# Kernel tuning notes

Measured on AMD Instinct MI355X. Metric: run time of the kernel, lower is better.

The kernel has to match this reference:

```python
import jax, jax.numpy as jnp
import numpy as np

B, K, NPER, Fin, Fmem, H = 64, 16, 256, 256, 128, 8
LN_EPS = 1e-5


def _build_edges():
    # each memory slot (src) attends over all K slots + NPER nodes of its batch elem
    BK = B * K
    dest_chunks = []
    for b in range(B):
        dest_b = np.concatenate([b * K + np.arange(K), BK + b * NPER + np.arange(NPER)])
        dest_chunks.append(np.tile(dest_b, K))
    dest = np.concatenate(dest_chunks).astype(np.int32)
    src = np.repeat(np.arange(BK), K + NPER).astype(np.int32)
    return src, dest


def setup_inputs() -> dict:
    key = jax.random.key(0)
    ks = jax.random.split(key, 16)
    N = B * NPER
    BK = B * K
    src, dest = _build_edges()
    s = 0.02
    return {
        'x': jax.random.normal(ks[0], (N, Fin), jnp.float32),
        'memory': jax.random.normal(ks[1], (BK, Fmem), jnp.float32),
        'Wp': jax.random.normal(ks[2], (Fin, Fmem), jnp.float32) * s,
        'bp': jnp.zeros((Fmem,), jnp.float32),
        'Wqkv': jax.random.normal(ks[3], (Fmem, 3 * Fmem), jnp.float32) * s,  # bias=False
        'ln1_g': jnp.ones((Fmem,), jnp.float32),
        'ln1_b': jnp.zeros((Fmem,), jnp.float32),
        'W1': jax.random.normal(ks[4], (Fmem, Fmem), jnp.float32) * s,
        'b1': jnp.zeros((Fmem,), jnp.float32),
        'W2': jax.random.normal(ks[5], (Fmem, Fmem), jnp.float32) * s,
        'b2': jnp.zeros((Fmem,), jnp.float32),
        'ln2_g': jnp.ones((Fmem,), jnp.float32),
        'ln2_b': jnp.zeros((Fmem,), jnp.float32),
        'Wg': jax.random.normal(ks[6], (2 * Fmem, 2 * Fmem), jnp.float32) * s,
        'bg': jnp.zeros((2 * Fmem,), jnp.float32),
        'src': jnp.asarray(src),
        'dest': jnp.asarray(dest),
    }


def layer_norm(x, g, b):
    mu = x.mean(-1, keepdims=True)
    var = ((x - mu) ** 2).mean(-1, keepdims=True)
    return (x - mu) * jax.lax.rsqrt(var + LN_EPS) * g + b


def reference(x, memory, Wp, bp, Wqkv, ln1_g, ln1_b, W1, b1, W2, b2,
              ln2_g, ln2_b, Wg, bg, src, dest):
    BK, F = memory.shape
    Fh = F // H
    # input projection and concat [memory; x]
    xp = x @ Wp + bp                               # [N, Fmem]
    mem_cat = jnp.concatenate([memory, xp], 0)     # [BK + N, Fmem]
    # qkv projection (no bias), Fqk = Fv = Fmem
    q, k, v = jnp.split(mem_cat @ Wqkv, 3, axis=-1)
    q = (q * (float(Fh) ** -0.5)).reshape(-1, H, Fh)
    k = k.reshape(-1, H, Fh)
    v = v.reshape(-1, H, Fh)
    # per-edge attention scores
    aw = jnp.einsum('ehf,ehf->eh', q[src], k[dest])          # [E, H]
    # scatter softmax over src segments
    m = jax.ops.segment_max(aw, src, num_segments=BK)
    e = jnp.exp(aw - m[src])
    z = jax.ops.segment_sum(e, src, num_segments=BK)
    p = e / z[src]                                            # [E, H]
    # weighted scatter-sum aggregation
    out = jax.ops.segment_sum(p[:, :, None] * v[dest], src, num_segments=BK)
    out = out.reshape(BK, F)
    # residual + LN, MLP, residual + LN
    mem_tmp = layer_norm(memory + out, ln1_g, ln1_b)
    mem_update = jax.nn.relu(mem_tmp @ W1 + b1) @ W2 + b2
    mem_update = layer_norm(mem_tmp + mem_update, ln2_g, ln2_b)
    # feature-level LSTM-style gating
    gate = jnp.concatenate([memory, mem_update], -1) @ Wg + bg
    f, i = jnp.split(gate, 2, axis=-1)
    new_mem = memory * jax.nn.sigmoid(f) + mem_update * jax.nn.sigmoid(i)
    return new_mem  # original returns (output, memory) with output is memory
```

## Files before the change

kernel.cpp:

```cpp
#include <hip/hip_runtime.h>
#include <hip/hip_bf16.h>

#define B_    64
#define K_    16
#define NPER_ 256
#define FIN_  256
#define F_    128
#define H_    8
#define N_    (B_ * NPER_)
#define BK_   (B_ * K_)
#define KV_   (K_ + NPER_)
#define LN_EPS_ 1e-5f

__device__ __forceinline__ float bf2f(unsigned short u) {
    union { unsigned u; float f; } c; c.u = ((unsigned)u) << 16; return c.f;
}
template<bool BF>
__device__ __forceinline__ float ldT(const void* p, long i) {
    if (BF) return bf2f(((const unsigned short*)p)[i]);
    else    return ((const float*)p)[i];
}
template<bool BF>
__device__ __forceinline__ float2 ld2T(const void* p, long i) {
    if (BF) {
        const unsigned u = *(const unsigned*)((const unsigned short*)p + i);
        return make_float2(bf2f((unsigned short)(u & 0xffffu)),
                           bf2f((unsigned short)(u >> 16)));
    } else {
        return *(const float2*)((const float*)p + i);
    }
}
template<bool BF>
__device__ __forceinline__ float4 ld4T(const void* p, long i) {
    if (BF) {
        const uint2 u = *(const uint2*)((const unsigned short*)p + i);
        return make_float4(bf2f((unsigned short)(u.x & 0xffffu)),
                           bf2f((unsigned short)(u.x >> 16)),
                           bf2f((unsigned short)(u.y & 0xffffu)),
                           bf2f((unsigned short)(u.y >> 16)));
    } else {
        return *(const float4*)((const float*)p + i);
    }
}
template<bool BF>
__device__ __forceinline__ void stT(void* p, long i, float v) {
    if (BF) ((__hip_bfloat16*)p)[i] = __float2bfloat16(v);
    else    ((float*)p)[i] = v;
}
__device__ __forceinline__ bool is_bf(const unsigned* probe) {
    return probe[0] != 0x3F800000u;
}

#define R1 32

template<bool BF>
__device__ __forceinline__ void stage_wp(const void* Wp, int c, float* dst, int t) {
    const long base = (long)c * 2048;
    *(float4*)(dst + 4 * t)        = ld4T<BF>(Wp, base + 4 * t);
    *(float4*)(dst + 1024 + 4 * t) = ld4T<BF>(Wp, base + 1024 + 4 * t);
}
template<bool BF>
__device__ __forceinline__ void stage_wkv(const void* Wqkv, int c, float* dst, int t) {
    #pragma unroll
    for (int p = 0; p < 2; ++p) {
        const int d = p * 1024 + 4 * t;
        const int rr = d >> 8, cc = d & 255;
        *(float4*)(dst + d) = ld4T<BF>(Wqkv, (long)(c * 8 + rr) * 384 + 128 + cc);
    }
}

template<bool BF>
__device__ void nodes_kv_body(const void* x, const void* Wp, const void* bp,
                              const void* Wqkv, float* kx, float* vx,
                              float* xs, float* xps, float* wb0, float* wb1) {
    const int t = threadIdx.x;
    const long row0 = (long)blockIdx.x * R1;
    #pragma unroll
    for (int p = 0; p < 8; ++p) {
        const int d = p * 1024 + 4 * t;
        *(float4*)(xs + d) = ld4T<BF>(x, row0 * FIN_ + d);
    }
    stage_wp<BF>(Wp, 0, wb0, t);
    __syncthreads();
    const int j2 = (t & 63) * 2;
    const int r0 = (t >> 6) * 8;
    {
        float a0[8], a1[8];
        #pragma unroll
        for (int r = 0; r < 8; ++r) { a0[r] = 0.f; a1[r] = 0.f; }
        for (int c = 0; c < 16; ++c) {
            const float* w = (c & 1) ? wb1 : wb0;
            if (c < 15) stage_wp<BF>(Wp, c + 1, (c & 1) ? wb0 : wb1, t);
            #pragma unroll
            for (int g = 0; g < 16; g += 4) {
                const float2 w0 = *(const float2*)(w + (g + 0) * F_ + j2);
                const float2 w1 = *(const float2*)(w + (g + 1) * F_ + j2);
                const float2 w2 = *(const float2*)(w + (g + 2) * F_ + j2);
                const float2 w3 = *(const float2*)(w + (g + 3) * F_ + j2);
                #pragma unroll
                for (int r = 0; r < 8; ++r) {
                    const float4 x4 = *(const float4*)(xs + (r0 + r) * FIN_ + c * 16 + g);
                    a0[r] += x4.x * w0.x + x4.y * w1.x + x4.z * w2.x + x4.w * w3.x;
                    a1[r] += x4.x * w0.y + x4.y * w1.y + x4.z * w2.y + x4.w * w3.y;
                }
            }
            __syncthreads();
        }
        stage_wkv<BF>(Wqkv, 0, wb0, t);
        const float2 bb = ld2T<BF>(bp, j2);
        #pragma unroll
        for (int r = 0; r < 8; ++r)
            *(float2*)(xps + (r0 + r) * F_ + j2) = make_float2(a0[r] + bb.x, a1[r] + bb.y);
    }
    __syncthreads();
    {
        float b0[8], b1[8], c0a[8], c1a[8];
        #pragma unroll
        for (int r = 0; r < 8; ++r) { b0[r] = b1[r] = c0a[r] = c1a[r] = 0.f; }
        for (int c = 0; c < 16; ++c) {
            const float* w = (c & 1) ? wb1 : wb0;
            if (c < 15) stage_wkv<BF>(Wqkv, c + 1, (c & 1) ? wb0 : wb1, t);
            #pragma unroll
            for (int g = 0; g < 8; g += 4) {
                const float2 wk0 = *(const float2*)(w + (g + 0) * 256 + j2);
                const float2 wk1 = *(const float2*)(w + (g + 1) * 256 + j2);
                const float2 wk2 = *(const float2*)(w + (g + 2) * 256 + j2);
                const float2 wk3 = *(const float2*)(w + (g + 3) * 256 + j2);
                const float2 wv0 = *(const float2*)(w + (g + 0) * 256 + 128 + j2);
                const float2 wv1 = *(const float2*)(w + (g + 1) * 256 + 128 + j2);
                const float2 wv2 = *(const float2*)(w + (g + 2) * 256 + 128 + j2);
                const float2 wv3 = *(const float2*)(w + (g + 3) * 256 + 128 + j2);
                #pragma unroll
                for (int r = 0; r < 8; ++r) {
                    const float4 p4 = *(const float4*)(xps + (r0 + r) * F_ + c * 8 + g);
                    b0[r]  += p4.x * wk0.x + p4.y * wk1.x + p4.z * wk2.x + p4.w * wk3.x;
                    b1[r]  += p4.x * wk0.y + p4.y * wk1.y + p4.z * wk2.y + p4.w * wk3.y;
                    c0a[r] += p4.x * wv0.x + p4.y * wv1.x + p4.z * wv2.x + p4.w * wv3.x;
                    c1a[r] += p4.x * wv0.y + p4.y * wv1.y + p4.z * wv2.y + p4.w * wv3.y;
                }
            }
            __syncthreads();
        }
        #pragma unroll
        for (int r = 0; r < 8; ++r) {
            const long g = (row0 + r0 + r) * F_;
            *(float2*)(kx + g + j2) = make_float2(b0[r], b1[r]);
            *(float2*)(vx + g + j2) = make_float2(c0a[r], c1a[r]);
        }
    }
}
__global__ __launch_bounds__(256) void k_nodes_kv(const void* x, const void* Wp,
        const void* bp, const void* Wqkv, const unsigned* probe,
        float* kx, float* vx) {
    __shared__ float xs[R1 * FIN_];
    __shared__ float xps[R1 * F_];
    __shared__ float wb0[2048];
    __shared__ float wb1[2048];
    if (is_bf(probe)) nodes_kv_body<true >(x, Wp, bp, Wqkv, kx, vx, xs, xps, wb0, wb1);
    else              nodes_kv_body<false>(x, Wp, bp, Wqkv, kx, vx, xs, xps, wb0, wb1);
}

#define KPAD 20
template<bool BF>
__device__ void attn_body(const void* mem, const void* Wqkv,
                          const float* kx, const float* vx, float* attn_out,
                          float* ms, float* qh, float* kh, float* vh, float* S) {
    const int b = blockIdx.x >> 3, h = blockIdx.x & 7;
    const int t = threadIdx.x;
    #pragma unroll
    for (int p = 0; p < 2; ++p) {
        const int d = p * 1024 + 4 * t;
        *(float4*)(ms + d) = ld4T<BF>(mem, (long)(b * 16) * F_ + d);
    }
    #pragma unroll
    for (int p = 0; p < 4; ++p) {
        const int i = t + p * 256;
        const int e = i >> 2, d4 = (i & 3) * 4;
        const long a = ((long)(b * NPER_) + e) * F_ + h * 16 + d4;
        *(float4*)(kh + (16 + e) * KPAD + d4) = *(const float4*)(kx + a);
        *(float4*)(vh + (16 + e) * KPAD + d4) = *(const float4*)(vx + a);
    }
    __syncthreads();
    {
        const int row = t >> 4, d = t & 15;
        float aq = 0.f, ak = 0.f, av = 0.f;
        const float* mr = ms + row * F_;
        for (int f = 0; f < F_; f += 4) {
            const float4 m4 = *(const float4*)(mr + f);
            float mm[4] = {m4.x, m4.y, m4.z, m4.w};
            #pragma unroll
            for (int q = 0; q < 4; ++q) {
                const long wrow = (long)(f + q) * 384 + h * 16 + d;
                aq += mm[q] * ldT<BF>(Wqkv, wrow);
                ak += mm[q] * ldT<BF>(Wqkv, wrow + 128);
                av += mm[q] * ldT<BF>(Wqkv, wrow + 256);
            }
        }
        qh[row * 16 + d]   = aq * 0.25f;
        kh[row * KPAD + d] = ak;
        vh[row * KPAD + d] = av;
    }
    __syncthreads();
    {
        const int e = t;
        float acc[16];
        #pragma unroll
        for (int r = 0; r < 16; ++r) acc[r] = 0.f;
        #pragma unroll
        for (int dq = 0; dq < 16; dq += 4) {
            const float4 k4 = *(const float4*)(kh + e * KPAD + dq);
            #pragma unroll
            for (int r = 0; r < 16; ++r) {
                const float4 q4 = *(const float4*)(qh + r * 16 + dq);
                acc[r] += q4.x * k4.x + q4.y * k4.y + q4.z * k4.z + q4.w * k4.w;
            }
        }
        #pragma unroll
        for (int r = 0; r < 16; ++r) S[r * KV_ + e] = acc[r];
        const int e2 = 256 + (t >> 4), r2 = t & 15;
        float a2 = 0.f;
        #pragma unroll
        for (int dq = 0; dq < 16; dq += 4) {
            const float4 k4 = *(const float4*)(kh + e2 * KPAD + dq);
            const float4 q4 = *(const float4*)(qh + r2 * 16 + dq);
            a2 += q4.x * k4.x + q4.y * k4.y + q4.z * k4.z + q4.w * k4.w;
        }
        S[r2 * KV_ + e2] = a2;
    }
    __syncthreads();
    {
        const int wave = t >> 6, lane = t & 63;
        for (int r = wave; r < 16; r += 4) {
            float m = -1e30f;
            for (int e = lane; e < KV_; e += 64) m = fmaxf(m, S[r * KV_ + e]);
            for (int off = 32; off; off >>= 1) m = fmaxf(m, __shfl_xor(m, off));
            float z = 0.f;
            for (int e = lane; e < KV_; e += 64) {
                const float p = __expf(S[r * KV_ + e] - m);
                S[r * KV_ + e] = p; z += p;
            }
            for (int off = 32; off; off >>= 1) z += __shfl_xor(z, off);
            const float inv = 1.f / z;
            for (int e = lane; e < KV_; e += 64) S[r * KV_ + e] *= inv;
        }
    }
    __syncthreads();
    {
        const int r = t >> 4, d = t & 15;
        float o0 = 0.f, o1 = 0.f, o2 = 0.f, o3 = 0.f;
        for (int e = 0; e < KV_; e += 4) {
            const float4 p4 = *(const float4*)(S + r * KV_ + e);
            o0 += p4.x * vh[(e + 0) * KPAD + d];
            o1 += p4.y * vh[(e + 1) * KPAD + d];
            o2 += p4.z * vh[(e + 2) * KPAD + d];
            o3 += p4.w * vh[(e + 3) * KPAD + d];
        }
        attn_out[((long)(b * 16) + r) * F_ + h * 16 + d] = (o0 + o1) + (o2 + o3);
    }
}
__global__ __launch_bounds__(256) void k_attn(const void* mem, const void* Wqkv,
        const float* kx, const float* vx, const unsigned* probe, float* attn_out) {
    __shared__ float ms[16 * F_];
    __shared__ float qh[16 * 16];
    __shared__ float kh[KV_ * KPAD];
    __shared__ float vh[KV_ * KPAD];
    __shared__ float S[16 * KV_];
    if (is_bf(probe)) attn_body<true >(mem, Wqkv, kx, vx, attn_out, ms, qh, kh, vh, S);
    else              attn_body<false>(mem, Wqkv, kx, vx, attn_out, ms, qh, kh, vh, S);
}

#define R4 2
template<bool BF>
__device__ void post_body(const void* mem, const float* attn,
                          const void* ln1g, const void* ln1b,
                          const void* W1, const void* b1,
                          const void* W2, const void* b2,
                          const void* ln2g, const void* ln2b,
                          const void* Wg, const void* bg,
                          void* out,
                          float* ms, float* hs, float* ts, float* cat, float* gs) {
    const int t = threadIdx.x;
    const int r0b = blockIdx.x * R4;
    if (t < 128) {
        const int rr = t >> 6, c0 = (t & 63) * 2;
        const long gbase = (long)(r0b + rr) * F_ + c0;
        const float mv0 = ldT<BF>(mem, gbase), mv1 = ldT<BF>(mem, gbase + 1);
        const float2 a2 = *(const float2*)(attn + gbase);
        const float y0 = mv0 + a2.x, y1 = mv1 + a2.y;
        float s = y0 + y1;
        #pragma unroll
        for (int off = 32; off; off >>= 1) s += __shfl_xor(s, off);
        const float mu = s * (1.f / 128.f);
        const float d0 = y0 - mu, d1 = y1 - mu;
        float v = d0 * d0 + d1 * d1;
        #pragma unroll
        for (int off = 32; off; off >>= 1) v += __shfl_xor(v, off);
        const float inv = rsqrtf(v * (1.f / 128.f) + LN_EPS_);
        ms[rr * F_ + c0]     = d0 * inv * ldT<BF>(ln1g, c0)     + ldT<BF>(ln1b, c0);
        ms[rr * F_ + c0 + 1] = d1 * inv * ldT<BF>(ln1g, c0 + 1) + ldT<BF>(ln1b, c0 + 1);
        cat[rr * 256 + c0]     = mv0;
        cat[rr * 256 + c0 + 1] = mv1;
    }
    __syncthreads();
    {
        const int r = t >> 7, j = t & 127;
        const float* mr = ms + r * F_;
        float p0 = 0.f, p1 = 0.f, p2 = 0.f, p3 = 0.f;
        for (int f = 0; f < F_; f += 8) {
            const float4 ma = *(const float4*)(mr + f);
            const float4 mb = *(const float4*)(mr + f + 4);
            p0 += ma.x * ldT<BF>(W1, (long)(f + 0) * F_ + j);
            p1 += ma.y * ldT<BF>(W1, (long)(f + 1) * F_ + j);
            p2 += ma.z * ldT<BF>(W1, (long)(f + 2) * F_ + j);
            p3 += ma.w * ldT<BF>(W1, (long)(f + 3) * F_ + j);
            p0 += mb.x * ldT<BF>(W1, (long)(f + 4) * F_ + j);
            p1 += mb.y * ldT<BF>(W1, (long)(f + 5) * F_ + j);
            p2 += mb.z * ldT<BF>(W1, (long)(f + 6) * F_ + j);
            p3 += mb.w * ldT<BF>(W1, (long)(f + 7) * F_ + j);
        }
        hs[r * F_ + j] = fmaxf((p0 + p1) + (p2 + p3) + ldT<BF>(b1, j), 0.f);
    }
    __syncthreads();
    {
        const int r = t >> 7, j = t & 127;
        const float* hr = hs + r * F_;
        float p0 = 0.f, p1 = 0.f, p2 = 0.f, p3 = 0.f;
        for (int f = 0; f < F_; f += 8) {
            const float4 ha = *(const float4*)(hr + f);
            const float4 hb = *(const float4*)(hr + f + 4);
            p0 += ha.x * ldT<BF>(W2, (long)(f + 0) * F_ + j);
            p1 += ha.y * ldT<BF>(W2, (long)(f + 1) * F_ + j);
            p2 += ha.z * ldT<BF>(W2, (long)(f + 2) * F_ + j);
            p3 += ha.w * ldT<BF>(W2, (long)(f + 3) * F_ + j);
            p0 += hb.x * ldT<BF>(W2, (long)(f + 4) * F_ + j);
            p1 += hb.y * ldT<BF>(W2, (long)(f + 5) * F_ + j);
            p2 += hb.z * ldT<BF>(W2, (long)(f + 6) * F_ + j);
            p3 += hb.w * ldT<BF>(W2, (long)(f + 7) * F_ + j);
        }
        ts[r * F_ + j] = ms[r * F_ + j] + (p0 + p1) + (p2 + p3) + ldT<BF>(b2, j);
    }
    __syncthreads();
    if (t < 128) {
        const int rr = t >> 6, c0 = (t & 63) * 2;
        const float z0 = ts[rr * F_ + c0], z1 = ts[rr * F_ + c0 + 1];
        float s = z0 + z1;
        #pragma unroll
        for (int off = 32; off; off >>= 1) s += __shfl_xor(s, off);
        const float mu = s * (1.f / 128.f);
        const float d0 = z0 - mu, d1 = z1 - mu;
        float v = d0 * d0 + d1 * d1;
        #pragma unroll
        for (int off = 32; off; off >>= 1) v += __shfl_xor(v, off);
        const float inv = rsqrtf(v * (1.f / 128.f) + LN_EPS_);
        cat[rr * 256 + 128 + c0]     = d0 * inv * ldT<BF>(ln2g, c0)     + ldT<BF>(ln2b, c0);
        cat[rr * 256 + 128 + c0 + 1] = d1 * inv * ldT<BF>(ln2g, c0 + 1) + ldT<BF>(ln2b, c0 + 1);
    }
    __syncthreads();
    {
        const int c = t;
        float q0 = 0.f, q1 = 0.f, q2 = 0.f, q3 = 0.f;
        for (int f = 0; f < 256; f += 4) {
            const float w0 = ldT<BF>(Wg, (long)(f + 0) * 256 + c);
            const float w1 = ldT<BF>(Wg, (long)(f + 1) * 256 + c);
            const float w2 = ldT<BF>(Wg, (long)(f + 2) * 256 + c);
            const float w3 = ldT<BF>(Wg, (long)(f + 3) * 256 + c);
            const float4 ca = *(const float4*)(cat + f);
            const float4 cb = *(const float4*)(cat + 256 + f);
            q0 += ca.x * w0 + ca.z * w2;
            q1 += ca.y * w1 + ca.w * w3;
            q2 += cb.x * w0 + cb.z * w2;
            q3 += cb.y * w1 + cb.w * w3;
        }
        const float bgc = ldT<BF>(bg, c);
        gs[c]       = (q0 + q1) + bgc;
        gs[256 + c] = (q2 + q3) + bgc;
    }
    __syncthreads();
    {
        const int r = t >> 7, cf = t & 127;
        const float gf = gs[r * 256 + cf], gi = gs[r * 256 + 128 + cf];
        const float m0 = cat[r * 256 + cf], uu = cat[r * 256 + 128 + cf];
        const float val = m0 * (1.f / (1.f + __expf(-gf)))
                        + uu * (1.f / (1.f + __expf(-gi)));
        stT<BF>(out, (long)(r0b + r) * F_ + cf, val);
    }
}
__global__ __launch_bounds__(256) void k_post(const void* mem, const float* attn,
        const void* ln1g, const void* ln1b, const void* W1, const void* b1,
        const void* W2, const void* b2, const void* ln2g, const void* ln2b,
        const void* Wg, const void* bg, const unsigned* probe, void* out) {
    __shared__ float ms[R4 * F_];
    __shared__ float hs[R4 * F_];
    __shared__ float ts[R4 * F_];
    __shared__ float cat[R4 * 2 * F_];
    __shared__ float gs[R4 * 2 * F_];
    if (is_bf(probe)) post_body<true >(mem, attn, ln1g, ln1b, W1, b1, W2, b2,
                                       ln2g, ln2b, Wg, bg, out, ms, hs, ts, cat, gs);
    else              post_body<false>(mem, attn, ln1g, ln1b, W1, b1, W2, b2,
                                       ln2g, ln2b, Wg, bg, out, ms, hs, ts, cat, gs);
}

extern "C" void kernel_launch(void* const* d_in, const int* in_sizes, int n_in,
                              void* d_out, int out_size, void* d_ws, size_t ws_size,
                              hipStream_t stream) {
    const void* x      = d_in[0];
    const void* memory = d_in[1];
    const void* Wp     = d_in[2];
    const void* bp     = d_in[3];
    const void* Wqkv   = d_in[4];
    const void* ln1g   = d_in[5];
    const void* ln1b   = d_in[6];
    const void* W1     = d_in[7];
    const void* b1     = d_in[8];
    const void* W2     = d_in[9];
    const void* b2     = d_in[10];
    const void* ln2g   = d_in[11];
    const void* ln2b   = d_in[12];
    const void* Wg     = d_in[13];
    const void* bg     = d_in[14];
    const unsigned* probe = (const unsigned*)d_in[5];

    float* ws   = (float*)d_ws;
    float* kx   = ws;
    float* vx   = kx + (long)N_ * F_;
    float* attn = vx + (long)N_ * F_;

    k_nodes_kv <<<N_ / R1, 256, 0, stream>>>(x, Wp, bp, Wqkv, probe, kx, vx);
    k_attn     <<<B_ * H_, 256, 0, stream>>>(memory, Wqkv, kx, vx, probe, attn);
    k_post     <<<BK_ / R4, 256, 0, stream>>>(memory, attn, ln1g, ln1b, W1, b1,
                                              W2, b2, ln2g, ln2b, Wg, bg, probe, d_out);
}
```

Measured before the change: 192.6 us.

## Use split-bf16 MFMA GEMMs for input and QKV projections, split post-kernel matvecs

Replaces the fused scalar-FP32 node projection kernel with two MFMA GEMM kernels. They emulate FP32 with a bf16 hi/lo split and three MFMAs per product. The memory-row QKV projection moves out of the attention kernel into the shared GEMM, and the post kernel's W1/W2/Wg matvecs split K across thread halves with wider vector weight loads. This adds an extra kernel launch and an xp round trip through global memory. The bf16x3 emulation drops the lo*lo term, so the results are only approximately FP32.

```diff
diff --git a/kernel.cpp b/kernel.cpp
--- a/kernel.cpp
+++ b/kernel.cpp
@@ -12,6 +12,9 @@
 #define KV_   (K_ + NPER_)
 #define LN_EPS_ 1e-5f
 
+typedef short short8v __attribute__((ext_vector_type(8)));
+typedef float float4v __attribute__((ext_vector_type(4)));
+
 __device__ __forceinline__ float bf2f(unsigned short u) {
     union { unsigned u; float f; } c; c.u = ((unsigned)u) << 16; return c.f;
 }
@@ -51,126 +54,205 @@
     return probe[0] != 0x3F800000u;
 }
 
-#define R1 32
-
-template<bool BF>
-__device__ __forceinline__ void stage_wp(const void* Wp, int c, float* dst, int t) {
-    const long base = (long)c * 2048;
-    *(float4*)(dst + 4 * t)        = ld4T<BF>(Wp, base + 4 * t);
-    *(float4*)(dst + 1024 + 4 * t) = ld4T<BF>(Wp, base + 1024 + 4 * t);
-}
-template<bool BF>
-__device__ __forceinline__ void stage_wkv(const void* Wqkv, int c, float* dst, int t) {
+__device__ __forceinline__ unsigned short f2bf_rne(float f) {
+    union { float f; unsigned u; } c; c.f = f;
+    const unsigned r = c.u + 0x7FFFu + ((c.u >> 16) & 1u);
+    return (unsigned short)(r >> 16);
+}
+__device__ __forceinline__ unsigned long long pack4(unsigned short a, unsigned short b,
+                                                    unsigned short c, unsigned short d) {
+    return (unsigned long long)a | ((unsigned long long)b << 16)
+         | ((unsigned long long)c << 32) | ((unsigned long long)d << 48);
+}
+
+#define LDK 40
+
+template<bool BF>
+__device__ void gemm_xp_body(const void* x, const void* Wp, const void* bp,
+                             float* xp, short* Ah, short* Al, short* Bh, short* Bl) {
+    const int t = threadIdx.x;
+    const int row0 = blockIdx.x * 32;
+    const int wave = t >> 6, lane = t & 63;
+    const int wm = wave >> 1, wn = wave & 1;
+    const int l15 = lane & 15, l4 = lane >> 4;
+    float4v acc[4];
     #pragma unroll
-    for (int p = 0; p < 2; ++p) {
-        const int d = p * 1024 + 4 * t;
-        const int rr = d >> 8, cc = d & 255;
-        *(float4*)(dst + d) = ld4T<BF>(Wqkv, (long)(c * 8 + rr) * 384 + 128 + cc);
-    }
-}
-
-template<bool BF>
-__device__ void nodes_kv_body(const void* x, const void* Wp, const void* bp,
-                              const void* Wqkv, float* kx, float* vx,
-                              float* xs, float* xps, float* wb0, float* wb1) {
+    for (int fc = 0; fc < 4; ++fc) acc[fc] = (float4v){0.f, 0.f, 0.f, 0.f};
+
+    for (int ks = 0; ks < 8; ++ks) {
+        const int k0 = ks * 32;
+        {
+            const int ar = t >> 3, kq = (t & 7) * 4;
+            const float4 v4 = ld4T<BF>(x, (long)(row0 + ar) * FIN_ + k0 + kq);
+            unsigned short h0 = f2bf_rne(v4.x), h1 = f2bf_rne(v4.y);
+            unsigned short h2 = f2bf_rne(v4.z), h3 = f2bf_rne(v4.w);
+            *(unsigned long long*)(Ah + ar * LDK + kq) = pack4(h0, h1, h2, h3);
+            *(unsigned long long*)(Al + ar * LDK + kq) = pack4(
+                f2bf_rne(v4.x - bf2f(h0)), f2bf_rne(v4.y - bf2f(h1)),
+                f2bf_rne(v4.z - bf2f(h2)), f2bf_rne(v4.w - bf2f(h3)));
+        }
+        {
+            const int j = t & 127, khh = (t >> 7) * 16;
+            unsigned short hh[16], ll[16];
+            #pragma unroll
+            for (int kk = 0; kk < 16; ++kk) {
+                const float w = ldT<BF>(Wp, (long)(k0 + khh + kk) * F_ + j);
+                hh[kk] = f2bf_rne(w);
+                ll[kk] = f2bf_rne(w - bf2f(hh[kk]));
+            }
+            #pragma unroll
+            for (int g = 0; g < 4; ++g) {
+                *(unsigned long long*)(Bh + j * LDK + khh + 4 * g) =
+                    pack4(hh[4*g], hh[4*g+1], hh[4*g+2], hh[4*g+3]);
+                *(unsigned long long*)(Bl + j * LDK + khh + 4 * g) =
+                    pack4(ll[4*g], ll[4*g+1], ll[4*g+2], ll[4*g+3]);
+            }
+        }
+        __syncthreads();
+        {
+            const int abase = (wm * 16 + l15) * LDK + 8 * l4;
+            const short8v ah = *(const short8v*)(Ah + abase);
+            const short8v al = *(const short8v*)(Al + abase);
+            #pragma unroll
+            for (int fc = 0; fc < 4; ++fc) {
+                const int bbase = (wn * 64 + fc * 16 + l15) * LDK + 8 * l4;
+                const short8v bh = *(const short8v*)(Bh + bbase);
+                const short8v bl = *(const short8v*)(Bl + bbase);
+                acc[fc] = __builtin_amdgcn_mfma_f32_16x16x32_bf16(ah, bh, acc[fc], 0, 0, 0);
+                acc[fc] = __builtin_amdgcn_mfma_f32_16x16x32_bf16(ah, bl, acc[fc], 0, 0, 0);
+                acc[fc] = __builtin_amdgcn_mfma_f32_16x16x32_bf16(al, bh, acc[fc], 0, 0, 0);
+            }
+        }
+        __syncthreads();
+    }
+    #pragma unroll
+    for (int fc = 0; fc < 4; ++fc) {
+        const int col = wn * 64 + fc * 16 + l15;
+        const float bb = ldT<BF>(bp, col);
+        #pragma unroll
+        for (int reg = 0; reg < 4; ++reg) {
+            const int row = row0 + wm * 16 + l4 * 4 + reg;
+            xp[(long)row * F_ + col] = acc[fc][reg] + bb;
+        }
+    }
+}
+__global__ __launch_bounds__(256) void k_gemm_xp(const void* x, const void* Wp,
+        const void* bp, const unsigned* probe, float* xp) {
+    __shared__ __align__(16) short Ah[32 * LDK];
+    __shared__ __align__(16) short Al[32 * LDK];
+    __shared__ __align__(16) short Bh[128 * LDK];
+    __shared__ __align__(16) short Bl[128 * LDK];
+    if (is_bf(probe)) gemm_xp_body<true >(x, Wp, bp, xp, Ah, Al, Bh, Bl);
+    else              gemm_xp_body<false>(x, Wp, bp, xp, Ah, Al, Bh, Bl);
+}
+
+template<bool BF>
+__device__ void gemm_qkv_body(const float* xp, const void* mem, const void* Wqkv,
+                              float* kx, float* vx, float* qm, float* km, float* vm,
+                              short* Ah, short* Al, short* Bh, short* Bl) {
+    const int mb = blockIdx.x, nb = blockIdx.y;
+    const bool isMem = (mb >= 512);
     const int t = threadIdx.x;
-    const long row0 = (long)blockIdx.x * R1;
+    const int wave = t >> 6, lane = t & 63;
+    const int wm = wave >> 1, wn = wave & 1;
+    const int l15 = lane & 15, l4 = lane >> 4;
+    float4v acc[4];
     #pragma unroll
-    for (int p = 0; p < 8; ++p) {
-        const int d = p * 1024 + 4 * t;
-        *(float4*)(xs + d) = ld4T<BF>(x, row0 * FIN_ + d);
-    }
-    stage_wp<BF>(Wp, 0, wb0, t);
-    __syncthreads();
-    const int j2 = (t & 63) * 2;
-    const int r0 = (t >> 6) * 8;
-    {
-        float a0[8], a1[8];
-        #pragma unroll
-        for (int r = 0; r < 8; ++r) { a0[r] = 0.f; a1[r] = 0.f; }
-        for (int c = 0; c < 16; ++c) {
-            const float* w = (c & 1) ? wb1 : wb0;
-            if (c < 15) stage_wp<BF>(Wp, c + 1, (c & 1) ? wb0 : wb1, t);
-            #pragma unroll
-            for (int g = 0; g < 16; g += 4) {
-                const float2 w0 = *(const float2*)(w + (g + 0) * F_ + j2);
-                const float2 w1 = *(const float2*)(w + (g + 1) * F_ + j2);
-                const float2 w2 = *(const float2*)(w + (g + 2) * F_ + j2);
-                const float2 w3 = *(const float2*)(w + (g + 3) * F_ + j2);
-                #pragma unroll
-                for (int r = 0; r < 8; ++r) {
-                    const float4 x4 = *(const float4*)(xs + (r0 + r) * FIN_ + c * 16 + g);
-                    a0[r] += x4.x * w0.x + x4.y * w1.x + x4.z * w2.x + x4.w * w3.x;
-                    a1[r] += x4.x * w0.y + x4.y * w1.y + x4.z * w2.y + x4.w * w3.y;
-                }
-            }
-            __syncthreads();
-        }
-        stage_wkv<BF>(Wqkv, 0, wb0, t);
-        const float2 bb = ld2T<BF>(bp, j2);
-        #pragma unroll
-        for (int r = 0; r < 8; ++r)
-            *(float2*)(xps + (r0 + r) * F_ + j2) = make_float2(a0[r] + bb.x, a1[r] + bb.y);
-    }
-    __syncthreads();
-    {
-        float b0[8], b1[8], c0a[8], c1a[8];
-        #pragma unroll
-        for (int r = 0; r < 8; ++r) { b0[r] = b1[r] = c0a[r] = c1a[r] = 0.f; }
-        for (int c = 0; c < 16; ++c) {
-            const float* w = (c & 1) ? wb1 : wb0;
-            if (c < 15) stage_wkv<BF>(Wqkv, c + 1, (c & 1) ? wb0 : wb1, t);
-            #pragma unroll
-            for (int g = 0; g < 8; g += 4) {
-                const float2 wk0 = *(const float2*)(w + (g + 0) * 256 + j2);
-                const float2 wk1 = *(const float2*)(w + (g + 1) * 256 + j2);
-                const float2 wk2 = *(const float2*)(w + (g + 2) * 256 + j2);
-                const float2 wk3 = *(const float2*)(w + (g + 3) * 256 + j2);
-                const float2 wv0 = *(const float2*)(w + (g + 0) * 256 + 128 + j2);
-                const float2 wv1 = *(const float2*)(w + (g + 1) * 256 + 128 + j2);
-                const float2 wv2 = *(const float2*)(w + (g + 2) * 256 + 128 + j2);
-                const float2 wv3 = *(const float2*)(w + (g + 3) * 256 + 128 + j2);
-                #pragma unroll
-                for (int r = 0; r < 8; ++r) {
-                    const float4 p4 = *(const float4*)(xps + (r0 + r) * F_ + c * 8 + g);
-                    b0[r]  += p4.x * wk0.x + p4.y * wk1.x + p4.z * wk2.x + p4.w * wk3.x;
-                    b1[r]  += p4.x * wk0.y + p4.y * wk1.y + p4.z * wk2.y + p4.w * wk3.y;
-                    c0a[r] += p4.x * wv0.x + p4.y * wv1.x + p4.z * wv2.x + p4.w * wv3.x;
-                    c1a[r] += p4.x * wv0.y + p4.y * wv1.y + p4.z * wv2.y + p4.w * wv3.y;
-                }
-            }
-            __syncthreads();
-        }
-        #pragma unroll
-        for (int r = 0; r < 8; ++r) {
-            const long g = (row0 + r0 + r) * F_;
-            *(float2*)(kx + g + j2) = make_float2(b0[r], b1[r]);
-            *(float2*)(vx + g + j2) = make_float2(c0a[r], c1a[r]);
-        }
-    }
-}
-__global__ __launch_bounds__(256) void k_nodes_kv(const void* x, const void* Wp,
-        const void* bp, const void* Wqkv, const unsigned* probe,
-        float* kx, float* vx) {
-    __shared__ float xs[R1 * FIN_];
-    __shared__ float xps[R1 * F_];
-    __shared__ float wb0[2048];
-    __shared__ float wb1[2048];
-    if (is_bf(probe)) nodes_kv_body<true >(x, Wp, bp, Wqkv, kx, vx, xs, xps, wb0, wb1);
-    else              nodes_kv_body<false>(x, Wp, bp, Wqkv, kx, vx, xs, xps, wb0, wb1);
+    for (int fc = 0; fc < 4; ++fc) acc[fc] = (float4v){0.f, 0.f, 0.f, 0.f};
+
+    for (int ks = 0; ks < 4; ++ks) {
+        const int k0 = ks * 32;
+        {
+            const int ar = t >> 3, kq = (t & 7) * 4;
+            float4 v4;
+            if (isMem) v4 = ld4T<BF>(mem, (long)((mb - 512) * 32 + ar) * F_ + k0 + kq);
+            else       v4 = *(const float4*)(xp + (long)(mb * 32 + ar) * F_ + k0 + kq);
+            unsigned short h0 = f2bf_rne(v4.x), h1 = f2bf_rne(v4.y);
+            unsigned short h2 = f2bf_rne(v4.z), h3 = f2bf_rne(v4.w);
+            *(unsigned long long*)(Ah + ar * LDK + kq) = pack4(h0, h1, h2, h3);
+            *(unsigned long long*)(Al + ar * LDK + kq) = pack4(
+                f2bf_rne(v4.x - bf2f(h0)), f2bf_rne(v4.y - bf2f(h1)),
+                f2bf_rne(v4.z - bf2f(h2)), f2bf_rne(v4.w - bf2f(h3)));
+        }
+        {
+            const int j = t & 127, khh = (t >> 7) * 16;
+            unsigned short hh[16], ll[16];
+            #pragma unroll
+            for (int kk = 0; kk < 16; ++kk) {
+                const float w = ldT<BF>(Wqkv, (long)(k0 + khh + kk) * 384 + nb * 128 + j);
+                hh[kk] = f2bf_rne(w);
+                ll[kk] = f2bf_rne(w - bf2f(hh[kk]));
+            }
+            #pragma unroll
+            for (int g = 0; g < 4; ++g) {
+                *(unsigned long long*)(Bh + j * LDK + khh + 4 * g) =
+                    pack4(hh[4*g], hh[4*g+1], hh[4*g+2], hh[4*g+3]);
+                *(unsigned long long*)(Bl + j * LDK + khh + 4 * g) =
+                    pack4(ll[4*g], ll[4*g+1], ll[4*g+2], ll[4*g+3]);
+            }
+        }
+        __syncthreads();
+        {
+            const int abase = (wm * 16 + l15) * LDK + 8 * l4;
+            const short8v ah = *(const short8v*)(Ah + abase);
+            const short8v al = *(const short8v*)(Al + abase);
+            #pragma unroll
+            for (int fc = 0; fc < 4; ++fc) {
+                const int bbase = (wn * 64 + fc * 16 + l15) * LDK + 8 * l4;
+                const short8v bh = *(const short8v*)(Bh + bbase);
+                const short8v bl = *(const short8v*)(Bl + bbase);
+                acc[fc] = __builtin_amdgcn_mfma_f32_16x16x32_bf16(ah, bh, acc[fc], 0, 0, 0);
+                acc[fc] = __builtin_amdgcn_mfma_f32_16x16x32_bf16(ah, bl, acc[fc], 0, 0, 0);
+                acc[fc] = __builtin_amdgcn_mfma_f32_16x16x32_bf16(al, bh, acc[fc], 0, 0, 0);
+            }
+        }
+        __syncthreads();
+    }
+    #pragma unroll
+    for (int fc = 0; fc < 4; ++fc) {
+        const int col = wn * 64 + fc * 16 + l15;
+        #pragma unroll
+        for (int reg = 0; reg < 4; ++reg) {
+            const int mrow = mb * 32 + wm * 16 + l4 * 4 + reg;
+            const float v = acc[fc][reg];
+            if (!isMem) {
+                ((nb == 1) ? kx : vx)[(long)mrow * F_ + col] = v;
+            } else {
+                const long s = mrow - 16384;
+                if      (nb == 0) qm[s * F_ + col] = v * 0.25f;
+                else if (nb == 1) km[s * F_ + col] = v;
+                else              vm[s * F_ + col] = v;
+            }
+        }
+    }
+}
+__global__ __launch_bounds__(256) void k_gemm_qkv(const float* xp, const void* mem,
+        const void* Wqkv, const unsigned* probe,
+        float* kx, float* vx, float* qm, float* km, float* vm) {
+    if (blockIdx.y == 0 && blockIdx.x < 512) return;
+    __shared__ __align__(16) short Ah[32 * LDK];
+    __shared__ __align__(16) short Al[32 * LDK];
+    __shared__ __align__(16) short Bh[128 * LDK];
+    __shared__ __align__(16) short Bl[128 * LDK];
+    if (is_bf(probe)) gemm_qkv_body<true >(xp, mem, Wqkv, kx, vx, qm, km, vm, Ah, Al, Bh, Bl);
+    else              gemm_qkv_body<false>(xp, mem, Wqkv, kx, vx, qm, km, vm, Ah, Al, Bh, Bl);
 }
 
 #define KPAD 20
-template<bool BF>
-__device__ void attn_body(const void* mem, const void* Wqkv,
-                          const float* kx, const float* vx, float* attn_out,
-                          float* ms, float* qh, float* kh, float* vh, float* S) {
+__global__ __launch_bounds__(256) void k_attn(const float* qm, const float* km,
+        const float* vm, const float* kx, const float* vx, float* attn_out) {
+    __shared__ float qh[16 * 16];
+    __shared__ float kh[KV_ * KPAD];
+    __shared__ float vh[KV_ * KPAD];
+    __shared__ float S[16 * KV_];
     const int b = blockIdx.x >> 3, h = blockIdx.x & 7;
     const int t = threadIdx.x;
-    #pragma unroll
-    for (int p = 0; p < 2; ++p) {
-        const int d = p * 1024 + 4 * t;
-        *(float4*)(ms + d) = ld4T<BF>(mem, (long)(b * 16) * F_ + d);
+    qh[t] = qm[(long)(b * 16 + (t >> 4)) * F_ + h * 16 + (t & 15)];
+    if (t < 64) {
+        const int e = t >> 2, d4 = (t & 3) * 4;
+        const long a = (long)(b * K_ + e) * F_ + h * 16 + d4;
+        *(float4*)(kh + e * KPAD + d4) = *(const float4*)(km + a);
+        *(float4*)(vh + e * KPAD + d4) = *(const float4*)(vm + a);
     }
     #pragma unroll
     for (int p = 0; p < 4; ++p) {
@@ -179,26 +261,6 @@
         const long a = ((long)(b * NPER_) + e) * F_ + h * 16 + d4;
         *(float4*)(kh + (16 + e) * KPAD + d4) = *(const float4*)(kx + a);
         *(float4*)(vh + (16 + e) * KPAD + d4) = *(const float4*)(vx + a);
-    }
-    __syncthreads();
-    {
-        const int row = t >> 4, d = t & 15;
-        float aq = 0.f, ak = 0.f, av = 0.f;
-        const float* mr = ms + row * F_;
-        for (int f = 0; f < F_; f += 4) {
-            const float4 m4 = *(const float4*)(mr + f);
-            float mm[4] = {m4.x, m4.y, m4.z, m4.w};
-            #pragma unroll
-            for (int q = 0; q < 4; ++q) {
-                const long wrow = (long)(f + q) * 384 + h * 16 + d;
-                aq += mm[q] * ldT<BF>(Wqkv, wrow);
-                ak += mm[q] * ldT<BF>(Wqkv, wrow + 128);
-                av += mm[q] * ldT<BF>(Wqkv, wrow + 256);
-            }
-        }
-        qh[row * 16 + d]   = aq * 0.25f;
-        kh[row * KPAD + d] = ak;
-        vh[row * KPAD + d] = av;
     }
     __syncthreads();
     {
@@ -258,16 +320,6 @@
         attn_out[((long)(b * 16) + r) * F_ + h * 16 + d] = (o0 + o1) + (o2 + o3);
     }
 }
-__global__ __launch_bounds__(256) void k_attn(const void* mem, const void* Wqkv,
-        const float* kx, const float* vx, const unsigned* probe, float* attn_out) {
-    __shared__ float ms[16 * F_];
-    __shared__ float qh[16 * 16];
-    __shared__ float kh[KV_ * KPAD];
-    __shared__ float vh[KV_ * KPAD];
-    __shared__ float S[16 * KV_];
-    if (is_bf(probe)) attn_body<true >(mem, Wqkv, kx, vx, attn_out, ms, qh, kh, vh, S);
-    else              attn_body<false>(mem, Wqkv, kx, vx, attn_out, ms, qh, kh, vh, S);
-}
 
 #define R4 2
 template<bool BF>
@@ -278,7 +330,8 @@
                           const void* ln2g, const void* ln2b,
                           const void* Wg, const void* bg,
                           void* out,
-                          float* ms, float* hs, float* ts, float* cat, float* gs) {
+                          float* ms, float* hs, float* ts, float* cat,
+                          float* gs, float (*pb)[R4][256]) {
     const int t = threadIdx.x;
     const int r0b = blockIdx.x * R4;
     if (t < 128) {
@@ -303,41 +356,53 @@
     }
     __syncthreads();
     {
-        const int r = t >> 7, j = t & 127;
-        const float* mr = ms + r * F_;
-        float p0 = 0.f, p1 = 0.f, p2 = 0.f, p3 = 0.f;
-        for (int f = 0; f < F_; f += 8) {
-            const float4 ma = *(const float4*)(mr + f);
-            const float4 mb = *(const float4*)(mr + f + 4);
-            p0 += ma.x * ldT<BF>(W1, (long)(f + 0) * F_ + j);
-            p1 += ma.y * ldT<BF>(W1, (long)(f + 1) * F_ + j);
-            p2 += ma.z * ldT<BF>(W1, (long)(f + 2) * F_ + j);
-            p3 += ma.w * ldT<BF>(W1, (long)(f + 3) * F_ + j);
-            p0 += mb.x * ldT<BF>(W1, (long)(f + 4) * F_ + j);
-            p1 += mb.y * ldT<BF>(W1, (long)(f + 5) * F_ + j);
-            p2 += mb.z * ldT<BF>(W1, (long)(f + 6) * F_ + j);
-            p3 += mb.w * ldT<BF>(W1, (long)(f + 7) * F_ + j);
-        }
-        hs[r * F_ + j] = fmaxf((p0 + p1) + (p2 + p3) + ldT<BF>(b1, j), 0.f);
-    }
-    __syncthreads();
-    {
-        const int r = t >> 7, j = t & 127;
-        const float* hr = hs + r * F_;
-        float p0 = 0.f, p1 = 0.f, p2 = 0.f, p3 = 0.f;
-        for (int f = 0; f < F_; f += 8) {
-            const float4 ha = *(const float4*)(hr + f);
-            const float4 hb = *(const float4*)(hr + f + 4);
-            p0 += ha.x * ldT<BF>(W2, (long)(f + 0) * F_ + j);
-            p1 += ha.y * ldT<BF>(W2, (long)(f + 1) * F_ + j);
-            p2 += ha.z * ldT<BF>(W2, (long)(f + 2) * F_ + j);
-            p3 += ha.w * ldT<BF>(W2, (long)(f + 3) * F_ + j);
-            p0 += hb.x * ldT<BF>(W2, (long)(f + 4) * F_ + j);
-            p1 += hb.y * ldT<BF>(W2, (long)(f + 5) * F_ + j);
-            p2 += hb.z * ldT<BF>(W2, (long)(f + 6) * F_ + j);
-            p3 += hb.w * ldT<BF>(W2, (long)(f + 7) * F_ + j);
-        }
-        ts[r * F_ + j] = ms[r * F_ + j] + (p0 + p1) + (p2 + p3) + ldT<BF>(b2, j);
+        const int jp2 = (t & 63) * 2, r = (t >> 6) & 1, kh = t >> 7;
+        const float* mr = ms + r * F_ + kh * 64;
+        float a0 = 0.f, a1 = 0.f, b0v = 0.f, b1v = 0.f;
+        #pragma unroll 4
+        for (int f = 0; f < 64; f += 4) {
+            const float4 m4 = *(const float4*)(mr + f);
+            const float2 w0 = ld2T<BF>(W1, (long)(kh * 64 + f + 0) * F_ + jp2);
+            const float2 w1 = ld2T<BF>(W1, (long)(kh * 64 + f + 1) * F_ + jp2);
+            const float2 w2 = ld2T<BF>(W1, (long)(kh * 64 + f + 2) * F_ + jp2);
+            const float2 w3 = ld2T<BF>(W1, (long)(kh * 64 + f + 3) * F_ + jp2);
+            a0  += m4.x * w0.x + m4.z * w2.x;
+            a1  += m4.y * w1.x + m4.w * w3.x;
+            b0v += m4.x * w0.y + m4.z * w2.y;
+            b1v += m4.y * w1.y + m4.w * w3.y;
+        }
+        pb[kh][r][jp2]     = a0 + a1;
+        pb[kh][r][jp2 + 1] = b0v + b1v;
+    }
+    __syncthreads();
+    {
+        const int r = t >> 7, c = t & 127;
+        hs[r * F_ + c] = fmaxf(pb[0][r][c] + pb[1][r][c] + ldT<BF>(b1, c), 0.f);
+    }
+    __syncthreads();
+    {
+        const int jp2 = (t & 63) * 2, r = (t >> 6) & 1, kh = t >> 7;
+        const float* hr = hs + r * F_ + kh * 64;
+        float a0 = 0.f, a1 = 0.f, b0v = 0.f, b1v = 0.f;
+        #pragma unroll 4
+        for (int f = 0; f < 64; f += 4) {
+            const float4 h4 = *(const float4*)(hr + f);
+            const float2 w0 = ld2T<BF>(W2, (long)(kh * 64 + f + 0) * F_ + jp2);
+            const float2 w1 = ld2T<BF>(W2, (long)(kh * 64 + f + 1) * F_ + jp2);
+            const float2 w2 = ld2T<BF>(W2, (long)(kh * 64 + f + 2) * F_ + jp2);
+            const float2 w3 = ld2T<BF>(W2, (long)(kh * 64 + f + 3) * F_ + jp2);
+            a0  += h4.x * w0.x + h4.z * w2.x;
+            a1  += h4.y * w1.x + h4.w * w3.x;
+            b0v += h4.x * w0.y + h4.z * w2.y;
+            b1v += h4.y * w1.y + h4.w * w3.y;
+        }
+        pb[kh][r][jp2]     = a0 + a1;
+        pb[kh][r][jp2 + 1] = b0v + b1v;
+    }
+    __syncthreads();
+    {
+        const int r = t >> 7, c = t & 127;
+        ts[r * F_ + c] = ms[r * F_ + c] + pb[0][r][c] + pb[1][r][c] + ldT<BF>(b2, c);
     }
     __syncthreads();
     if (t < 128) {
@@ -357,23 +422,32 @@
     }
     __syncthreads();
     {
-        const int c = t;
-        float q0 = 0.f, q1 = 0.f, q2 = 0.f, q3 = 0.f;
-        for (int f = 0; f < 256; f += 4) {
-            const float w0 = ldT<BF>(Wg, (long)(f + 0) * 256 + c);
-            const float w1 = ldT<BF>(Wg, (long)(f + 1) * 256 + c);
-            const float w2 = ldT<BF>(Wg, (long)(f + 2) * 256 + c);
-            const float w3 = ldT<BF>(Wg, (long)(f + 3) * 256 + c);
-            const float4 ca = *(const float4*)(cat + f);
-            const float4 cb = *(const float4*)(cat + 256 + f);
-            q0 += ca.x * w0 + ca.z * w2;
-            q1 += ca.y * w1 + ca.w * w3;
-            q2 += cb.x * w0 + cb.z * w2;
-            q3 += cb.y * w1 + cb.w * w3;
-        }
-        const float bgc = ldT<BF>(bg, c);
-        gs[c]       = (q0 + q1) + bgc;
-        gs[256 + c] = (q2 + q3) + bgc;
+        const int cq4 = (t & 63) * 4, r = (t >> 6) & 1, kh = t >> 7;
+        const float* cr = cat + r * 256 + kh * 128;
+        float a0 = 0.f, a1 = 0.f, a2 = 0.f, a3 = 0.f;
+        #pragma unroll 2
+        for (int f = 0; f < 128; f += 4) {
+            const float4 c4 = *(const float4*)(cr + f);
+            float4 w;
+            w = ld4T<BF>(Wg, (long)(kh * 128 + f + 0) * 256 + cq4);
+            a0 += c4.x * w.x; a1 += c4.x * w.y; a2 += c4.x * w.z; a3 += c4.x * w.w;
+            w = ld4T<BF>(Wg, (long)(kh * 128 + f + 1) * 256 + cq4);
+            a0 += c4.y * w.x; a1 += c4.y * w.y; a2 += c4.y * w.z; a3 += c4.y * w.w;
+            w = ld4T<BF>(Wg, (long)(kh * 128 + f + 2) * 256 + cq4);
+            a0 += c4.z * w.x; a1 += c4.z * w.y; a2 += c4.z * w.z; a3 += c4.z * w.w;
+            w = ld4T<BF>(Wg, (long)(kh * 128 + f + 3) * 256 + cq4);
+            a0 += c4.w * w.x; a1 += c4.w * w.y; a2 += c4.w * w.z; a3 += c4.w * w.w;
+        }
+        pb[kh][r][cq4 + 0] = a0; pb[kh][r][cq4 + 1] = a1;
+        pb[kh][r][cq4 + 2] = a2; pb[kh][r][cq4 + 3] = a3;
+    }
+    __syncthreads();
+    {
+        #pragma unroll
+        for (int o = t; o < 512; o += 256) {
+            const int r = o >> 8, c = o & 255;
+            gs[r * 256 + c] = pb[0][r][c] + pb[1][r][c] + ldT<BF>(bg, c);
+        }
     }
     __syncthreads();
     {
@@ -394,10 +468,11 @@
     __shared__ float ts[R4 * F_];
     __shared__ float cat[R4 * 2 * F_];
     __shared__ float gs[R4 * 2 * F_];
+    __shared__ float pb[2][R4][256];
     if (is_bf(probe)) post_body<true >(mem, attn, ln1g, ln1b, W1, b1, W2, b2,
-                                       ln2g, ln2b, Wg, bg, out, ms, hs, ts, cat, gs);
+                                       ln2g, ln2b, Wg, bg, out, ms, hs, ts, cat, gs, pb);
     else              post_body<false>(mem, attn, ln1g, ln1b, W1, b1, W2, b2,
-                                       ln2g, ln2b, Wg, bg, out, ms, hs, ts, cat, gs);
+                                       ln2g, ln2b, Wg, bg, out, ms, hs, ts, cat, gs, pb);
 }
 
 extern "C" void kernel_launch(void* const* d_in, const int* in_sizes, int n_in,
@@ -421,12 +496,18 @@
     const unsigned* probe = (const unsigned*)d_in[5];
 
     float* ws   = (float*)d_ws;
-    float* kx   = ws;
+    float* xp   = ws;
+    float* kx   = xp + (long)N_ * F_;
     float* vx   = kx + (long)N_ * F_;
-    float* attn = vx + (long)N_ * F_;
-
-    k_nodes_kv <<<N_ / R1, 256, 0, stream>>>(x, Wp, bp, Wqkv, probe, kx, vx);
-    k_attn     <<<B_ * H_, 256, 0, stream>>>(memory, Wqkv, kx, vx, probe, attn);
+    float* qm   = vx + (long)N_ * F_;
+    float* km   = qm + (long)BK_ * F_;
+    float* vm   = km + (long)BK_ * F_;
+    float* attn = vm + (long)BK_ * F_;
+
+    k_gemm_xp  <<<N_ / 32, 256, 0, stream>>>(x, Wp, bp, probe, xp);
+    k_gemm_qkv <<<dim3((N_ + BK_) / 32, 3), 256, 0, stream>>>(xp, memory, Wqkv, probe,
+                                                              kx, vx, qm, km, vm);
+    k_attn     <<<B_ * H_, 256, 0, stream>>>(qm, km, vm, kx, vx, attn);
     k_post     <<<BK_ / R4, 256, 0, stream>>>(memory, attn, ln1g, ln1b, W1, b1,
                                               W2, b2, ln2g, ln2b, Wg, bg, probe, d_out);
 }
```

Result: faster. 155.0 us (-19.5%).
